# Kernel tuning notes

Hardware: AMD Instinct MI355X
Metric: run time of the kernel (lower is better)

## Reference

```python
import jax, jax.numpy as jnp
import numpy as np

B, L, D, H = 2, 2048, 512, 8
DK = D // H


def setup_inputs() -> dict:
    key = jax.random.key(0)
    ks = jax.random.split(key, 10)
    s = 1.0 / np.sqrt(D)  # keep pre-softmax logits O(1)
    E = jax.random.normal(ks[0], (B, L, D), jnp.float32)
    Ev = jax.random.normal(ks[1], (B, L, D), jnp.float32)
    # R exactly as matrixR(L+1, D): sinusoid table transposed -> (D, L)
    inv_freq = 1.0 / (10000.0 ** (jnp.arange(0.0, D, 2.0) / D))
    sin_inp = jnp.arange(L, dtype=jnp.float32)[:, None] * inv_freq[None, :]
    R = jnp.concatenate([jnp.sin(sin_inp), jnp.cos(sin_inp)], axis=-1).T
    Wq = jax.random.normal(ks[2], (D, D), jnp.float32) * s
    Wke = jax.random.normal(ks[3], (D, D), jnp.float32) * s
    Wv = jax.random.normal(ks[4], (D, D), jnp.float32) * s
    Wkr = jax.random.normal(ks[5], (D, D), jnp.float32) * s
    cb = jax.random.normal(ks[6], (D,), jnp.float32) * 0.02
    pb = jax.random.normal(ks[7], (D,), jnp.float32) * 0.02
    Wo_w = jax.random.normal(ks[8], (D, D), jnp.float32) * s
    Wo_b = jnp.zeros((D,), jnp.float32)
    ln_g = jnp.ones((D,), jnp.float32)
    ln_b = jnp.zeros((D,), jnp.float32)
    return {"E": E, "Ev": Ev, "R": R, "Wq": Wq, "Wke": Wke, "Wv": Wv,
            "Wkr": Wkr, "cb": cb, "pb": pb, "Wo_w": Wo_w, "Wo_b": Wo_b,
            "ln_g": ln_g, "ln_b": ln_b}


def _shift(b):
    # Transformer-XL shift trick: pad one zero column, reinterpret rows.
    Bn, Hn, Ln, Mn = b.shape
    z = jnp.zeros((Bn, Hn, Ln, 1), b.dtype)
    bp = jnp.concatenate([z, b], axis=3).reshape(Bn, Hn, Mn + 1, Ln)
    return bp[:, :, 1:, :].reshape(Bn, Hn, Ln, Mn)[:, :, :, :Ln]


def reference(E, Ev, R, Wq, Wke, Wv, Wkr, cb, pb, Wo_w, Wo_b, ln_g, ln_b):
    Bn, Ln, Dn = E.shape
    q = (E @ Wq).reshape(Bn, Ln, H, DK).transpose(0, 2, 1, 3)   # (B,H,L,DK)
    k = (E @ Wke).reshape(Bn, Ln, H, DK).transpose(0, 2, 1, 3)  # (B,H,L,DK)
    v = (Ev @ Wv).reshape(Bn, Ln, H, DK).transpose(0, 2, 1, 3)  # (B,H,L,DK)
    Q = (Wkr @ R).reshape(1, H, DK, Ln)                          # (1,H,DK,L)
    kT = jnp.swapaxes(k, -2, -1)                                 # (B,H,DK,L)
    Bsc = q @ Q                                                  # (B,H,L,L)
    Dsc = jnp.broadcast_to(pb.reshape(1, H, 1, DK) @ Q, (Bn, H, Ln, Ln))
    A = (q @ kT) + _shift(Bsc) + (cb.reshape(1, H, 1, DK) @ kT) + _shift(Dsc)
    p = jax.nn.softmax(A, axis=-1)
    Oh = p @ v                                                   # (B,H,L,DK)
    O = Oh.reshape(Bn, Ln, Dn)  # faithful to torch view (no head transpose back)
    y = Ev + O @ Wo_w.T + Wo_b
    mu = jnp.mean(y, axis=-1, keepdims=True)
    var = jnp.var(y, axis=-1, keepdims=True)
    return (y - mu) / jnp.sqrt(var + 1e-5) * ln_g + ln_b
```

## Files before the change

kernel.cpp:

```cpp
#include <hip/hip_runtime.h>
#include <hip/hip_bf16.h>

#define Lc   2048
#define Dc   512
#define Hc   8
#define DKc  64
#define Bc   2
#define NSPLIT 4
#define BHLc (Bc*Hc*Lc)

typedef __attribute__((ext_vector_type(8))) short bf16x8;
typedef __attribute__((ext_vector_type(4))) float f32x4;
typedef __attribute__((ext_vector_type(4))) int   i32x4;
typedef unsigned short u16;

#define MFMA16(a, b, c) __builtin_amdgcn_mfma_f32_16x16x32_bf16((a), (b), (c), 0, 0, 0)

__device__ __forceinline__ u16 f2bf(float x) {
    union { float f; unsigned u; } v; v.f = x;
    unsigned r = v.u + 0x7FFFu + ((v.u >> 16) & 1u);
    return (u16)(r >> 16);
}
__device__ __forceinline__ float bf2f(u16 x) {
    union { unsigned u; float f; } v; v.u = ((unsigned)x) << 16; return v.f;
}

union U16x8 { u16 us[8]; i32x4 v; };

template<int TRANS>
__device__ __forceinline__ void stage_tile(u16* sDst, const float* __restrict__ src,
                                           int r0, int k0, int ld, int t)
{
    if (!TRANS) {
        const int row = t >> 2, q = t & 3;
        const float* s = src + (size_t)(r0 + row) * ld + k0 + q * 16;
        float4 f0 = ((const float4*)s)[0];
        float4 f1 = ((const float4*)s)[1];
        float4 f2 = ((const float4*)s)[2];
        float4 f3 = ((const float4*)s)[3];
        U16x8 a, b;
        a.us[0]=f2bf(f0.x); a.us[1]=f2bf(f0.y); a.us[2]=f2bf(f0.z); a.us[3]=f2bf(f0.w);
        a.us[4]=f2bf(f1.x); a.us[5]=f2bf(f1.y); a.us[6]=f2bf(f1.z); a.us[7]=f2bf(f1.w);
        b.us[0]=f2bf(f2.x); b.us[1]=f2bf(f2.y); b.us[2]=f2bf(f2.z); b.us[3]=f2bf(f2.w);
        b.us[4]=f2bf(f3.x); b.us[5]=f2bf(f3.y); b.us[6]=f2bf(f3.z); b.us[7]=f2bf(f3.w);
        const int r7 = row & 7, base = row * 64;
        *(i32x4*)&sDst[base + (((q*2)     ^ r7) << 3)] = a.v;
        *(i32x4*)&sDst[base + (((q*2 + 1) ^ r7) << 3)] = b.v;
    } else {
        const int qq = t & 31, mg = t >> 5;
        const float* s0 = src + (size_t)(k0 + 2*qq) * ld + r0 + mg*8;
        const float* s1 = s0 + ld;
        float4 x0 = ((const float4*)s0)[0], x1 = ((const float4*)s0)[1];
        float4 y0 = ((const float4*)s1)[0], y1 = ((const float4*)s1)[1];
        float e0[8] = {x0.x,x0.y,x0.z,x0.w,x1.x,x1.y,x1.z,x1.w};
        float e1[8] = {y0.x,y0.y,y0.z,y0.w,y1.x,y1.y,y1.z,y1.w};
        unsigned* d32 = (unsigned*)sDst;
        const int g = qq >> 2, off = qq & 3;
#pragma unroll
        for (int e = 0; e < 8; ++e) {
            const int m = mg*8 + e;
            unsigned pk = (unsigned)f2bf(e0[e]) | ((unsigned)f2bf(e1[e]) << 16);
            d32[m*32 + ((g ^ (m & 7)) << 2) + off] = pk;
        }
    }
}

template<int AT, int WT, int OUTMODE, int DUAL, int HASBIAS, int ADDSRC, int ABF = 0>
__global__ __launch_bounds__(256)
void gemm_mfma(const float* __restrict__ A, const float* __restrict__ W,
               const float* __restrict__ b1, const float* __restrict__ b2,
               const float* __restrict__ add, void* __restrict__ o1v,
               void* __restrict__ o2v, int ldA)
{
    __shared__ __align__(16) u16 sA[64*64];
    __shared__ __align__(16) u16 sB[64*64];
    const int m0 = blockIdx.x * 64, n0 = blockIdx.y * 64;
    const int t = threadIdx.x, lane = t & 63, w = t >> 6;
    const int l15 = lane & 15, lg = lane >> 4;
    const int wm = w >> 1, wn = w & 1;

    f32x4 acc[2][2] = {};

    for (int k0 = 0; k0 < 512; k0 += 64) {
        __syncthreads();
        if (ABF) {
            const u16* A16 = (const u16*)A;
            const int row = t >> 2, q = t & 3;
            const u16* s = A16 + (size_t)(m0 + row) * 512 + k0 + q*16;
            i32x4 v0 = ((const i32x4*)s)[0];
            i32x4 v1 = ((const i32x4*)s)[1];
            const int r7 = row & 7, base = row * 64;
            *(i32x4*)&sA[base + (((q*2)     ^ r7) << 3)] = v0;
            *(i32x4*)&sA[base + (((q*2 + 1) ^ r7) << 3)] = v1;
        } else {
            stage_tile<AT>(sA, A, m0, k0, AT ? ldA : 512, t);
        }
        stage_tile<WT ? 0 : 1>(sB, W, n0, k0, 512, t);
        __syncthreads();
        const int l7 = l15 & 7;
#pragma unroll
        for (int kh = 0; kh < 2; ++kh) {
            bf16x8 av[2], bv[2];
#pragma unroll
            for (int f = 0; f < 2; ++f) {
                const int ra = wm*32 + f*16 + l15;
                av[f] = *(const bf16x8*)&sA[ra*64 + (((kh*4 + lg) ^ l7) << 3)];
                const int rb = wn*32 + f*16 + l15;
                bv[f] = *(const bf16x8*)&sB[rb*64 + (((kh*4 + lg) ^ l7) << 3)];
            }
#pragma unroll
            for (int fm = 0; fm < 2; ++fm)
#pragma unroll
                for (int fn = 0; fn < 2; ++fn)
                    acc[fm][fn] = MFMA16(av[fm], bv[fn], acc[fm][fn]);
        }
    }

#pragma unroll
    for (int fm = 0; fm < 2; ++fm)
#pragma unroll
    for (int fn = 0; fn < 2; ++fn) {
        const int colg = n0 + wn*32 + fn*16 + l15;
#pragma unroll
        for (int r = 0; r < 4; ++r) {
            const int row = m0 + wm*32 + fm*16 + lg*4 + r;
            float v = acc[fm][fn][r];
            if (OUTMODE == 0) {
                if (HASBIAS) v += b1[colg];
                if (ADDSRC)  v += add[(size_t)row*512 + colg];
                ((float*)o1v)[(size_t)row*512 + colg] = v;
            } else if (OUTMODE == 1) {
                if (HASBIAS) v += b1[colg];
                const int h = colg >> 6, dk = colg & 63;
                const int bb = row >> 11, ii = row & 2047;
                const size_t idx = (((size_t)(bb*Hc + h)*Lc + ii) << 6) + dk;
                ((u16*)o1v)[idx] = f2bf(v);
                if (DUAL)
                    ((u16*)o2v)[idx] = f2bf(acc[fm][fn][r] + b2[colg]);
            } else if (OUTMODE == 2) {
                const int h = row >> 6, dk = row & 63;
                const int bb = colg >> 11, ii = colg & 2047;
                ((u16*)o1v)[((size_t)(bb*Hc + h)*DKc + dk)*Lc + ii] = f2bf(v);
            } else {
                const int h = colg >> 6, dk = colg & 63;
                ((u16*)o1v)[(((size_t)h*Lc + row) << 6) + dk] = f2bf(v);
            }
        }
    }
}

__global__ __launch_bounds__(256)
void gemm_qkp(const float* __restrict__ E, const float* __restrict__ Wq,
              const float* __restrict__ Wke, const float* __restrict__ cb,
              const float* __restrict__ pb, u16* __restrict__ qcB,
              u16* __restrict__ qpB, u16* __restrict__ kB)
{
    __shared__ __align__(16) u16 sA[64*64];
    __shared__ __align__(16) u16 sB1[64*64];
    __shared__ __align__(16) u16 sB2[64*64];
    const int m0 = blockIdx.x * 64, n0 = blockIdx.y * 64;
    const int t = threadIdx.x, lane = t & 63, w = t >> 6;
    const int l15 = lane & 15, lg = lane >> 4;
    const int wm = w >> 1, wn = w & 1;

    f32x4 acc1[2][2] = {};
    f32x4 acc2[2][2] = {};

    for (int k0 = 0; k0 < 512; k0 += 64) {
        __syncthreads();
        stage_tile<0>(sA,  E,   m0, k0, 512, t);
        stage_tile<1>(sB1, Wq,  n0, k0, 512, t);
        stage_tile<1>(sB2, Wke, n0, k0, 512, t);
        __syncthreads();
        const int l7 = l15 & 7;
#pragma unroll
        for (int kh = 0; kh < 2; ++kh) {
            bf16x8 av[2], b1v[2], b2v[2];
#pragma unroll
            for (int f = 0; f < 2; ++f) {
                const int ra = wm*32 + f*16 + l15;
                av[f]  = *(const bf16x8*)&sA [ra*64 + (((kh*4 + lg) ^ l7) << 3)];
                const int rb = wn*32 + f*16 + l15;
                b1v[f] = *(const bf16x8*)&sB1[rb*64 + (((kh*4 + lg) ^ l7) << 3)];
                b2v[f] = *(const bf16x8*)&sB2[rb*64 + (((kh*4 + lg) ^ l7) << 3)];
            }
#pragma unroll
            for (int fm = 0; fm < 2; ++fm)
#pragma unroll
                for (int fn = 0; fn < 2; ++fn) {
                    acc1[fm][fn] = MFMA16(av[fm], b1v[fn], acc1[fm][fn]);
                    acc2[fm][fn] = MFMA16(av[fm], b2v[fn], acc2[fm][fn]);
                }
        }
    }

#pragma unroll
    for (int fm = 0; fm < 2; ++fm)
#pragma unroll
    for (int fn = 0; fn < 2; ++fn) {
        const int colg = n0 + wn*32 + fn*16 + l15;
        const int h = colg >> 6, dk = colg & 63;
#pragma unroll
        for (int r = 0; r < 4; ++r) {
            const int row = m0 + wm*32 + fm*16 + lg*4 + r;
            const int bb = row >> 11, ii = row & 2047;
            const size_t idx = (((size_t)(bb*Hc + h)*Lc + ii) << 6) + dk;
            qcB[idx] = f2bf(acc1[fm][fn][r] + cb[colg]);
            qpB[idx] = f2bf(acc1[fm][fn][r] + pb[colg]);
            kB[idx]  = f2bf(acc2[fm][fn][r]);
        }
    }
}

__global__ __launch_bounds__(256, 4)
void attn_mfma(const u16* __restrict__ qc, const u16* __restrict__ qp,
               const u16* __restrict__ kk, const u16* __restrict__ vt,
               const u16* __restrict__ qrt, u16* __restrict__ Opart,
               float* __restrict__ mlbuf)
{
    __shared__ __align__(16) u16 sK[64*64];
    __shared__ __align__(16) u16 sV[64*64];
    __shared__ __align__(16) u16 sBand[128*64];
    __shared__ __align__(16) float sP2[4*1344];

    const int orig = ((blockIdx.x & 7) << 8) | (blockIdx.x >> 3);
    const int it = orig & 31;
    const int sp = (orig >> 5) & (NSPLIT - 1);
    const int bh = orig >> 7;
    const int h = bh & 7, b = bh >> 3;
    const int i0 = it << 6;
    const int t = threadIdx.x;
    const int lane = t & 63, w = t >> 6;
    const int l15 = lane & 15, lg = lane >> 4;

    float* p2w = sP2 + w * 1344;
    u16*   spw = (u16*)p2w;

    const size_t ho = (size_t)(b*Hc + h) * (Lc * DKc);
    const u16* qcH  = qc  + ho;
    const u16* qpH  = qp  + ho;
    const u16* kH   = kk  + ho;
    const u16* vtH  = vt  + ho;
    const u16* qrtH = qrt + (size_t)h * (Lc * DKc);

    const int rowA = i0 + w*16 + l15;
    const int rowB = (rowA + 1 < Lc) ? rowA + 1 : Lc - 1;
    bf16x8 qc0 = *(const bf16x8*)(qcH + (size_t)rowA*64 +      lg*8);
    bf16x8 qc1 = *(const bf16x8*)(qcH + (size_t)rowA*64 + 32 + lg*8);
    bf16x8 qa0 = *(const bf16x8*)(qpH + (size_t)rowA*64 +      lg*8);
    bf16x8 qa1 = *(const bf16x8*)(qpH + (size_t)rowA*64 + 32 + lg*8);
    bf16x8 qb0 = *(const bf16x8*)(qpH + (size_t)rowB*64 +      lg*8);
    bf16x8 qb1 = *(const bf16x8*)(qpH + (size_t)rowB*64 + 32 + lg*8);

    f32x4 oacc[4] = {};
    float mrow[4] = {-1e30f, -1e30f, -1e30f, -1e30f};
    float lsum[4] = {0.f, 0.f, 0.f, 0.f};

    for (int jq = 0; jq < 32/NSPLIT; ++jq) {
        const int jt = sp * (32/NSPLIT) + jq;
        const int j0 = jt << 6;
        const int dBase = j0 - i0 - 63;
        __syncthreads();
#pragma unroll
        for (int p = 0; p < 2; ++p) {
            const int s = t + p*256, row = s >> 3, g = s & 7;
            const int sl = row*64 + ((g ^ (row & 7)) << 3);
            *(i32x4*)&sK[sl] = *(const i32x4*)(kH  + (size_t)(j0+row)*64 + g*8);
            *(i32x4*)&sV[sl] = *(const i32x4*)(vtH + (size_t)row*Lc + j0 + g*8);
        }
#pragma unroll
        for (int p = 0; p < 4; ++p) {
            const int s = t + p*256, dd = s >> 3, g = s & 7;
            const int d = dBase + dd;
            const int m = (d <= 0) ? (d + Lc - 1) : ((d >= 2) ? (d - 2) : 0);
            *(i32x4*)&sBand[dd*64 + ((g ^ (dd & 7)) << 3)] =
                *(const i32x4*)(qrtH + (size_t)m*64 + g*8);
        }
        __syncthreads();

        __builtin_amdgcn_s_setprio(1);
        f32x4 sc[4];
#pragma unroll
        for (int nb = 0; nb < 4; ++nb) {
            const int row = nb*16 + l15;
            bf16x8 k0 = *(const bf16x8*)&sK[row*64 + ((( lg    ) ^ (row & 7)) << 3)];
            bf16x8 k1 = *(const bf16x8*)&sK[row*64 + (((lg + 4) ^ (row & 7)) << 3)];
            f32x4 z = {0.f, 0.f, 0.f, 0.f};
            z = MFMA16(qc0, k0, z);
            z = MFMA16(qc1, k1, z);
            sc[nb] = z;
        }

#pragma unroll
        for (int cbl = 0; cbl < 5; ++cbl) {
            const int cb  = cbl + 3 - w;
            const int row = cb*16 + l15;
            bf16x8 b0 = *(const bf16x8*)&sBand[row*64 + ((( lg    ) ^ (row & 7)) << 3)];
            bf16x8 b1 = *(const bf16x8*)&sBand[row*64 + (((lg + 4) ^ (row & 7)) << 3)];
            f32x4 z = {0.f, 0.f, 0.f, 0.f};
            if ((dBase + cb*16) >= 1) {
                z = MFMA16(qb0, b0, z);
                z = MFMA16(qb1, b1, z);
            } else {
                z = MFMA16(qa0, b0, z);
                z = MFMA16(qa1, b1, z);
            }
            if (!(cbl == 4 && l15 == 15)) {
                const int base = (cbl*16 + l15)*17 + lg*4;
                p2w[base+0] = z[0]; p2w[base+1] = z[1];
                p2w[base+2] = z[2]; p2w[base+3] = z[3];
            }
        }
        __builtin_amdgcn_s_setprio(0);
        __asm__ volatile("" ::: "memory");

        float pm[4];
#pragma unroll
        for (int r = 0; r < 4; ++r) {
            const int blm = lg*4 + r;
            const int blg = w*16 + blm;
#pragma unroll
            for (int nb = 0; nb < 4; ++nb) {
                const int jl = nb*16 + l15;
                const int d  = dBase + jl - blg + 63;
                const float pv = p2w[(jl - blm + 15)*17 + blm];
                sc[nb][r] += (d == 1) ? 0.f : pv;
            }
            pm[r] = fmaxf(fmaxf(sc[0][r], sc[1][r]), fmaxf(sc[2][r], sc[3][r]));
        }

        const float over = fmaxf(fmaxf(pm[0]-mrow[0], pm[1]-mrow[1]),
                                 fmaxf(pm[2]-mrow[2], pm[3]-mrow[3]));
        if (__all(over <= 8.0f)) {
#pragma unroll
            for (int r = 0; r < 4; ++r) {
                float p0 = __expf(sc[0][r] - mrow[r]);
                float p1 = __expf(sc[1][r] - mrow[r]);
                float p2 = __expf(sc[2][r] - mrow[r]);
                float p3 = __expf(sc[3][r] - mrow[r]);
                sc[0][r] = p0; sc[1][r] = p1; sc[2][r] = p2; sc[3][r] = p3;
                lsum[r] += p0 + p1 + p2 + p3;
            }
        } else {
            float fsc[4];
#pragma unroll
            for (int r = 0; r < 4; ++r) {
                float mx = pm[r];
                mx = fmaxf(mx, __shfl_xor(mx, 1, 64));
                mx = fmaxf(mx, __shfl_xor(mx, 2, 64));
                mx = fmaxf(mx, __shfl_xor(mx, 4, 64));
                mx = fmaxf(mx, __shfl_xor(mx, 8, 64));
                const float mnew = fmaxf(mrow[r], mx);
                const float fac  = __expf(mrow[r] - mnew);
                mrow[r] = mnew;
                float p0 = __expf(sc[0][r] - mnew);
                float p1 = __expf(sc[1][r] - mnew);
                float p2 = __expf(sc[2][r] - mnew);
                float p3 = __expf(sc[3][r] - mnew);
                sc[0][r] = p0; sc[1][r] = p1; sc[2][r] = p2; sc[3][r] = p3;
                lsum[r] = lsum[r] * fac + (p0 + p1 + p2 + p3);
                fsc[r] = fac;
            }
#pragma unroll
            for (int nb = 0; nb < 4; ++nb)
#pragma unroll
                for (int r = 0; r < 4; ++r)
                    oacc[nb][r] *= fsc[r];
        }
        __asm__ volatile("" ::: "memory");

#pragma unroll
        for (int r = 0; r < 4; ++r) {
            const int blm = lg*4 + r;
#pragma unroll
            for (int nb = 0; nb < 4; ++nb) {
                const int jl = nb*16 + l15;
                spw[blm*64 + (((jl >> 3) ^ (blm & 7)) << 3) + (jl & 7)] = f2bf(sc[nb][r]);
            }
        }
        __asm__ volatile("" ::: "memory");

        __builtin_amdgcn_s_setprio(1);
        {
            bf16x8 pa0 = *(const bf16x8*)&spw[l15*64 + ((( lg    ) ^ (l15 & 7)) << 3)];
            bf16x8 pa1 = *(const bf16x8*)&spw[l15*64 + (((lg + 4) ^ (l15 & 7)) << 3)];
#pragma unroll
            for (int nb = 0; nb < 4; ++nb) {
                const int row = nb*16 + l15;
                bf16x8 v0 = *(const bf16x8*)&sV[row*64 + ((( lg    ) ^ (row & 7)) << 3)];
                bf16x8 v1 = *(const bf16x8*)&sV[row*64 + (((lg + 4) ^ (row & 7)) << 3)];
                oacc[nb] = MFMA16(pa0, v0, oacc[nb]);
                oacc[nb] = MFMA16(pa1, v1, oacc[nb]);
            }
        }
        __builtin_amdgcn_s_setprio(0);
    }

    u16* Op = Opart + (size_t)sp * (Bc*Hc*Lc*DKc) + ho;
#pragma unroll
    for (int r = 0; r < 4; ++r) {
        float ls = lsum[r];
        ls += __shfl_xor(ls, 1, 64);
        ls += __shfl_xor(ls, 2, 64);
        ls += __shfl_xor(ls, 4, 64);
        ls += __shfl_xor(ls, 8, 64);
        const int bl = w*16 + lg*4 + r;
#pragma unroll
        for (int nb = 0; nb < 4; ++nb)
            Op[(size_t)(i0 + bl)*64 + nb*16 + l15] = f2bf(oacc[nb][r]);
        if (l15 == 0) {
            const int rglob = (b*Hc + h)*Lc + i0 + bl;
            *(float2*)&mlbuf[((size_t)sp*BHLc + rglob)*2] = make_float2(mrow[r], ls);
        }
    }
}

__global__ __launch_bounds__(256)
void attn_combine(const u16* __restrict__ Opart, const float* __restrict__ mlbuf,
                  u16* __restrict__ Oh)
{
    const int t = threadIdx.x;
    const int row = blockIdx.x * 64 + (t >> 2);
    const int q = t & 3;
    const size_t NQl = (size_t)Bc * Hc * Lc * DKc;

    float m[NSPLIT], l[NSPLIT];
#pragma unroll
    for (int s = 0; s < NSPLIT; ++s) {
        float2 ml = *(const float2*)&mlbuf[((size_t)s*BHLc + row)*2];
        m[s] = ml.x; l[s] = ml.y;
    }
    float M = fmaxf(fmaxf(m[0], m[1]), fmaxf(m[2], m[3]));
    float wgt[NSPLIT], wsum = 0.f;
#pragma unroll
    for (int s = 0; s < NSPLIT; ++s) { wgt[s] = __expf(m[s] - M); wsum += l[s]*wgt[s]; }
    const float inv = 1.f / wsum;

    float acc[16] = {};
#pragma unroll
    for (int s = 0; s < NSPLIT; ++s) {
        const i32x4* src = (const i32x4*)(Opart + (size_t)s*NQl + (size_t)row*64 + q*16);
        U16x8 a, b; a.v = src[0]; b.v = src[1];
#pragma unroll
        for (int e = 0; e < 8; ++e) {
            acc[e]   += wgt[s] * bf2f(a.us[e]);
            acc[8+e] += wgt[s] * bf2f(b.us[e]);
        }
    }
    U16x8 o0, o1;
#pragma unroll
    for (int e = 0; e < 8; ++e) {
        o0.us[e] = f2bf(acc[e]   * inv);
        o1.us[e] = f2bf(acc[8+e] * inv);
    }
    i32x4* dst = (i32x4*)(Oh + (size_t)row*64 + q*16);
    dst[0] = o0.v; dst[1] = o1.v;
}

__global__ __launch_bounds__(256)
void ln_kernel(const float* __restrict__ yr, const float* __restrict__ g,
               const float* __restrict__ be, float* __restrict__ out)
{
    const int row = blockIdx.x;
    const int t   = threadIdx.x;
    const float2 v = *(const float2*)&yr[(size_t)row * 512 + t*2];
    float sum = v.x + v.y;
    float sq  = v.x*v.x + v.y*v.y;
#pragma unroll
    for (int off = 1; off < 64; off <<= 1) {
        sum += __shfl_xor(sum, off, 64);
        sq  += __shfl_xor(sq,  off, 64);
    }
    __shared__ float ssum[4], ssq[4];
    if ((t & 63) == 0) { ssum[t >> 6] = sum; ssq[t >> 6] = sq; }
    __syncthreads();
    sum = ssum[0] + ssum[1] + ssum[2] + ssum[3];
    sq  = ssq[0]  + ssq[1]  + ssq[2]  + ssq[3];
    const float mu   = sum * (1.f / 512.f);
    const float var  = sq * (1.f / 512.f) - mu * mu;
    const float rstd = rsqrtf(var + 1e-5f);
    float2 ov;
    ov.x = (v.x - mu) * rstd * g[t*2+0] + be[t*2+0];
    ov.y = (v.y - mu) * rstd * g[t*2+1] + be[t*2+1];
    *(float2*)&out[(size_t)row * 512 + t*2] = ov;
}

extern "C" void kernel_launch(void* const* d_in, const int* in_sizes, int n_in,
                              void* d_out, int out_size, void* d_ws, size_t ws_size,
                              hipStream_t stream)
{
    const float* E    = (const float*)d_in[0];
    const float* Ev   = (const float*)d_in[1];
    const float* R    = (const float*)d_in[2];
    const float* Wq   = (const float*)d_in[3];
    const float* Wke  = (const float*)d_in[4];
    const float* Wv   = (const float*)d_in[5];
    const float* Wkr  = (const float*)d_in[6];
    const float* cb   = (const float*)d_in[7];
    const float* pb   = (const float*)d_in[8];
    const float* Wo_w = (const float*)d_in[9];
    const float* Wo_b = (const float*)d_in[10];
    const float* ln_g = (const float*)d_in[11];
    const float* ln_b = (const float*)d_in[12];
    float* out = (float*)d_out;

    const size_t NQ = (size_t)Bc * Hc * Lc * DKc;
    const size_t NR = (size_t)Hc * Lc * DKc;
    const size_t need = (4*NQ + NR)*2 + (size_t)NSPLIT*NQ*2 + (size_t)NSPLIT*BHLc*2*4;
    if (ws_size < need) return;

    u16* qcB  = (u16*)d_ws;
    u16* qpB  = qcB + NQ;
    u16* kB   = qpB + NQ;
    u16* vtB  = kB  + NQ;
    u16* qrtB = vtB + NQ;
    u16* Opart = qrtB + NR;
    float* mlbuf = (float*)(Opart + (size_t)NSPLIT*NQ);
    u16* Oh16 = Opart;
    float* yr = (float*)(Opart + NQ);

    dim3 blk(256);
    gemm_qkp<<<dim3(64,8), blk, 0, stream>>>(E, Wq, Wke, cb, pb, qcB, qpB, kB);
    gemm_mfma<1,1,2,0,0,0><<<dim3(8,64), blk, 0, stream>>>(Wv, Ev, nullptr, nullptr, nullptr, vtB, nullptr, 512);
    gemm_mfma<1,1,3,0,0,0><<<dim3(32,8), blk, 0, stream>>>(R, Wkr, nullptr, nullptr, nullptr, qrtB, nullptr, 2048);
    attn_mfma<<<dim3(Bc*Hc*NSPLIT*32), blk, 0, stream>>>(qcB, qpB, kB, vtB, qrtB, Opart, mlbuf);
    attn_combine<<<dim3(BHLc/64), blk, 0, stream>>>(Opart, mlbuf, Oh16);
    gemm_mfma<0,1,0,0,1,1,1><<<dim3(64,8), blk, 0, stream>>>((const float*)Oh16, Wo_w, Wo_b, nullptr, Ev, yr, nullptr, 512);
    ln_kernel<<<dim3(4096), blk, 0, stream>>>(yr, ln_g, ln_b, out);
}
```

Measured before the change: 169.2 us.

## Reuse relative-position band across key tiles via ring buffer; compact score scratch

Turns the shared-memory band of relative-position rows into a 128-slot ring buffer indexed by diagonal offset. The first key tile loads the full band, and each later tile loads only the 64 rows that are new, roughly halving global traffic for that table. The per-warp scratch for positional scores now stores the skewed values directly in a row-major 16x68 layout instead of a padded transposed one. This shrinks LDS use, which may allow more resident blocks per CU. The cost is extra index arithmetic and predicated scattered LDS stores, which may cause bank conflicts.

```diff
diff --git a/kernel.cpp b/kernel.cpp
--- a/kernel.cpp
+++ b/kernel.cpp
@@ -221,7 +221,7 @@
     __shared__ __align__(16) u16 sK[64*64];
     __shared__ __align__(16) u16 sV[64*64];
     __shared__ __align__(16) u16 sBand[128*64];
-    __shared__ __align__(16) float sP2[4*1344];
+    __shared__ __align__(16) float sP2[4*1088];
 
     const int orig = ((blockIdx.x & 7) << 8) | (blockIdx.x >> 3);
     const int it = orig & 31;
@@ -233,7 +233,7 @@
     const int lane = t & 63, w = t >> 6;
     const int l15 = lane & 15, lg = lane >> 4;
 
-    float* p2w = sP2 + w * 1344;
+    float* p2w = sP2 + w * 1088;
     u16*   spw = (u16*)p2w;
 
     const size_t ho = (size_t)(b*Hc + h) * (Lc * DKc);
@@ -268,13 +268,26 @@
             *(i32x4*)&sK[sl] = *(const i32x4*)(kH  + (size_t)(j0+row)*64 + g*8);
             *(i32x4*)&sV[sl] = *(const i32x4*)(vtH + (size_t)row*Lc + j0 + g*8);
         }
-#pragma unroll
-        for (int p = 0; p < 4; ++p) {
-            const int s = t + p*256, dd = s >> 3, g = s & 7;
-            const int d = dBase + dd;
-            const int m = (d <= 0) ? (d + Lc - 1) : ((d >= 2) ? (d - 2) : 0);
-            *(i32x4*)&sBand[dd*64 + ((g ^ (dd & 7)) << 3)] =
-                *(const i32x4*)(qrtH + (size_t)m*64 + g*8);
+        if (jq == 0) {
+#pragma unroll
+            for (int p = 0; p < 4; ++p) {
+                const int s = t + p*256, idx = s >> 3, g = s & 7;
+                const int d = dBase + idx;
+                const int m = (d <= 0) ? (d + Lc - 1) : ((d >= 2) ? (d - 2) : 0);
+                const int slot = (d + 2048) & 127;
+                *(i32x4*)&sBand[slot*64 + ((g ^ (slot & 7)) << 3)] =
+                    *(const i32x4*)(qrtH + (size_t)m*64 + g*8);
+            }
+        } else {
+#pragma unroll
+            for (int p = 0; p < 2; ++p) {
+                const int s = t + p*256, idx = s >> 3, g = s & 7;
+                const int d = dBase + 63 + idx;
+                const int m = (d <= 0) ? (d + Lc - 1) : ((d >= 2) ? (d - 2) : 0);
+                const int slot = (d + 2048) & 127;
+                *(i32x4*)&sBand[slot*64 + ((g ^ (slot & 7)) << 3)] =
+                    *(const i32x4*)(qrtH + (size_t)m*64 + g*8);
+            }
         }
         __syncthreads();
 
@@ -294,9 +307,10 @@
 #pragma unroll
         for (int cbl = 0; cbl < 5; ++cbl) {
             const int cb  = cbl + 3 - w;
-            const int row = cb*16 + l15;
-            bf16x8 b0 = *(const bf16x8*)&sBand[row*64 + ((( lg    ) ^ (row & 7)) << 3)];
-            bf16x8 b1 = *(const bf16x8*)&sBand[row*64 + (((lg + 4) ^ (row & 7)) << 3)];
+            const int d   = dBase + cb*16 + l15;
+            const int slot = (d + 2048) & 127;
+            bf16x8 b0 = *(const bf16x8*)&sBand[slot*64 + ((( lg    ) ^ (slot & 7)) << 3)];
+            bf16x8 b1 = *(const bf16x8*)&sBand[slot*64 + (((lg + 4) ^ (slot & 7)) << 3)];
             f32x4 z = {0.f, 0.f, 0.f, 0.f};
             if ((dBase + cb*16) >= 1) {
                 z = MFMA16(qb0, b0, z);
@@ -305,10 +319,11 @@
                 z = MFMA16(qa0, b0, z);
                 z = MFMA16(qa1, b1, z);
             }
-            if (!(cbl == 4 && l15 == 15)) {
-                const int base = (cbl*16 + l15)*17 + lg*4;
-                p2w[base+0] = z[0]; p2w[base+1] = z[1];
-                p2w[base+2] = z[2]; p2w[base+3] = z[3];
+#pragma unroll
+            for (int r = 0; r < 4; ++r) {
+                const int blm = lg*4 + r;
+                const int c = cbl*16 + l15 + blm - 15;
+                if ((unsigned)c < 64u) p2w[blm*68 + c] = z[r];
             }
         }
         __builtin_amdgcn_s_setprio(0);
@@ -323,7 +338,7 @@
             for (int nb = 0; nb < 4; ++nb) {
                 const int jl = nb*16 + l15;
                 const int d  = dBase + jl - blg + 63;
-                const float pv = p2w[(jl - blm + 15)*17 + blm];
+                const float pv = p2w[blm*68 + jl];
                 sc[nb][r] += (d == 1) ? 0.f : pv;
             }
             pm[r] = fmaxf(fmaxf(sc[0][r], sc[1][r]), fmaxf(sc[2][r], sc[3][r]));
```

New measurement: 172.5 us. 1.02x slower.
